# Optimization experiments

Hardware: AMD Instinct MI355X
Metric: run time of the kernel (lower is better)

## Reference

```python
import jax, jax.numpy as jnp
import numpy as np

H = 1024        # hidden_size
V = 50257       # output_size (vocab)
L = 50          # max_length (encoder positions)
N_LAYERS = 2    # python loop count over the shared single-layer GRU


def setup_inputs() -> dict:
    key = jax.random.key(0)
    ks = jax.random.split(key, 16)
    s = 0.02
    return {
        "input_ids": jax.random.randint(ks[0], (1,), 0, V),
        "hidden": jax.random.normal(ks[1], (1, 1, H), jnp.float32),
        "encoder_outputs": jax.random.normal(ks[2], (L, H), jnp.float32),
        # learned parameters
        "emb": jax.random.normal(ks[3], (V, H), jnp.float32) * s,
        "attn_w": jax.random.normal(ks[4], (L, 2 * H), jnp.float32) * s,
        "attn_b": jnp.zeros((L,), jnp.float32),
        "comb_w": jax.random.normal(ks[5], (H, 2 * H), jnp.float32) * s,
        "comb_b": jnp.zeros((H,), jnp.float32),
        "w_ih": jax.random.normal(ks[6], (3 * H, H), jnp.float32) * s,
        "w_hh": jax.random.normal(ks[7], (3 * H, H), jnp.float32) * s,
        "b_ih": jnp.zeros((3 * H,), jnp.float32),
        "b_hh": jnp.zeros((3 * H,), jnp.float32),
        "out_w": jax.random.normal(ks[8], (V, H), jnp.float32) * s,
        "out_b": jnp.zeros((V,), jnp.float32),
    }


def _gru_cell(x, h, w_ih, w_hh, b_ih, b_hh):
    # PyTorch GRU gate order: [r, z, n] stacked along dim 0 of (3H, H) weights.
    gx = w_ih @ x + b_ih
    gh = w_hh @ h + b_hh
    r = jax.nn.sigmoid(gx[:H] + gh[:H])
    z = jax.nn.sigmoid(gx[H:2 * H] + gh[H:2 * H])
    n = jnp.tanh(gx[2 * H:] + r * gh[2 * H:])
    return (1.0 - z) * n + z * h


def reference(input_ids, hidden, encoder_outputs, emb, attn_w, attn_b,
              comb_w, comb_b, w_ih, w_hh, b_ih, b_hh, out_w, out_b):
    # batch=1 single decode step; dropout is identity (eval mode)
    embedded = emb[input_ids[0]]                     # [H]
    h = hidden[0, 0]                                 # [H]
    concat = jnp.concatenate([embedded, h])          # [2H]
    attn_weights = jax.nn.softmax(attn_w @ concat + attn_b)   # [L]
    attn_applied = attn_weights @ encoder_outputs    # [H]  (bmm with batch 1)
    output = comb_w @ jnp.concatenate([embedded, attn_applied]) + comb_b  # [H]
    for _ in range(N_LAYERS):                        # shared-weight GRU called twice
        x = jax.nn.relu(output)
        h = _gru_cell(x, h, w_ih, w_hh, b_ih, b_hh)
        output = h
    log_probs = jax.nn.log_softmax(out_w @ output + out_b)    # [V]
    return log_probs[None, :], h[None, None, :], attn_weights[None, :]
```

## Files before the change

### kernel.cpp

```cpp
#include <hip/hip_runtime.h>
#include <hip/hip_bf16.h>

#define H 1024
#define V 50257
#define L 50

__global__ void scores_kernel(const int* __restrict__ input_ids,
                              const float* __restrict__ hidden,
                              const float* __restrict__ emb,
                              const float* __restrict__ attn_w,
                              const float* __restrict__ attn_b,
                              float* __restrict__ ws_scores) {
    __shared__ float s_part[8];
    const int tid = threadIdx.x;
    const int l   = blockIdx.x;
    const int wave = tid >> 6, lane = tid & 63;
    const int token = input_ids[0];

    float4 a = ((const float4*)(attn_w + (size_t)l * 2 * H))[tid];
    float4 x = (tid < 256) ? ((const float4*)(emb + (size_t)token * H))[tid]
                           : ((const float4*)hidden)[tid - 256];
    float acc = a.x * x.x + a.y * x.y + a.z * x.z + a.w * x.w;
    #pragma unroll
    for (int off = 32; off; off >>= 1) acc += __shfl_down(acc, off);
    if (lane == 0) s_part[wave] = acc;
    __syncthreads();
    if (tid == 0) {
        float s = 0.f;
        #pragma unroll
        for (int w = 0; w < 8; ++w) s += s_part[w];
        ws_scores[l] = s + attn_b[l];
    }
}

__global__ void applied_kernel(const float* __restrict__ ws_scores,
                               const float* __restrict__ enc,
                               float* __restrict__ ws_app,
                               float* __restrict__ out_attnw) {
    const int j = blockIdx.x * 256 + threadIdx.x;
    float w[L];
    float m = ws_scores[0];
    #pragma unroll
    for (int l = 1; l < L; ++l) m = fmaxf(m, ws_scores[l]);
    float s = 0.f;
    #pragma unroll
    for (int l = 0; l < L; ++l) { w[l] = expf(ws_scores[l] - m); s += w[l]; }
    float inv = 1.f / s;
    float acc = 0.f;
    #pragma unroll
    for (int l = 0; l < L; ++l) { w[l] *= inv; acc += w[l] * enc[l * H + j]; }
    ws_app[j] = acc;
    if (blockIdx.x == 0 && threadIdx.x < L) out_attnw[threadIdx.x] = w[threadIdx.x];
}

__global__ void comb_kernel(const float* __restrict__ comb_w,
                            const float* __restrict__ comb_b,
                            const int* __restrict__ input_ids,
                            const float* __restrict__ emb,
                            const float* __restrict__ applied,
                            float* __restrict__ x1) {
    __shared__ __align__(16) float s_c[2 * H];
    const int tid = threadIdx.x;
    const int token = input_ids[0];
    ((float4*)s_c)[tid] = ((const float4*)(emb + (size_t)token * H))[tid];
    ((float4*)(s_c + H))[tid] = ((const float4*)applied)[tid];
    __syncthreads();

    const int wave = tid >> 6, lane = tid & 63;
    const int i = blockIdx.x * 4 + wave;
    const float4* r4 = (const float4*)(comb_w + (size_t)i * 2 * H);
    const float4* c4 = (const float4*)s_c;
    float acc = 0.f;
    #pragma unroll
    for (int kk = 0; kk < 8; ++kk) {
        int k = kk * 64 + lane;
        float4 a = r4[k], b = c4[k];
        acc += a.x * b.x + a.y * b.y + a.z * b.z + a.w * b.w;
    }
    #pragma unroll
    for (int off = 32; off; off >>= 1) acc += __shfl_down(acc, off);
    if (lane == 0) x1[i] = fmaxf(acc + comb_b[i], 0.f);
}

__global__ void gru_kernel(const float* __restrict__ x,
                           const float* __restrict__ hprev,
                           const float* __restrict__ w_ih,
                           const float* __restrict__ w_hh,
                           const float* __restrict__ b_ih,
                           const float* __restrict__ b_hh,
                           float* __restrict__ h_out,
                           float* __restrict__ x_out,
                           float* __restrict__ h_copy)
{
    __shared__ __align__(16) float s_x[H];
    __shared__ __align__(16) float s_h[H];
    const int tid = threadIdx.x;
    ((float4*)s_x)[tid] = ((const float4*)x)[tid];
    ((float4*)s_h)[tid] = ((const float4*)hprev)[tid];
    __syncthreads();

    const int wave = tid >> 6, lane = tid & 63;
    const int i = blockIdx.x * 4 + wave;
    const float4* x4 = (const float4*)s_x;
    const float4* h4 = (const float4*)s_h;
    const float4* wr_x = (const float4*)(w_ih + (size_t)i * H);
    const float4* wz_x = (const float4*)(w_ih + (size_t)(H + i) * H);
    const float4* wn_x = (const float4*)(w_ih + (size_t)(2 * H + i) * H);
    const float4* wr_h = (const float4*)(w_hh + (size_t)i * H);
    const float4* wz_h = (const float4*)(w_hh + (size_t)(H + i) * H);
    const float4* wn_h = (const float4*)(w_hh + (size_t)(2 * H + i) * H);

    float ar = 0.f, az = 0.f, an = 0.f, br = 0.f, bz = 0.f, bn = 0.f;
    #pragma unroll
    for (int kk = 0; kk < 4; ++kk) {
        int k = kk * 64 + lane;
        float4 xv = x4[k], hv = h4[k], t;
        t = wr_x[k]; ar += t.x * xv.x + t.y * xv.y + t.z * xv.z + t.w * xv.w;
        t = wz_x[k]; az += t.x * xv.x + t.y * xv.y + t.z * xv.z + t.w * xv.w;
        t = wn_x[k]; an += t.x * xv.x + t.y * xv.y + t.z * xv.z + t.w * xv.w;
        t = wr_h[k]; br += t.x * hv.x + t.y * hv.y + t.z * hv.z + t.w * hv.w;
        t = wz_h[k]; bz += t.x * hv.x + t.y * hv.y + t.z * hv.z + t.w * hv.w;
        t = wn_h[k]; bn += t.x * hv.x + t.y * hv.y + t.z * hv.z + t.w * hv.w;
    }
    #pragma unroll
    for (int off = 32; off; off >>= 1) {
        ar += __shfl_down(ar, off); az += __shfl_down(az, off);
        an += __shfl_down(an, off); br += __shfl_down(br, off);
        bz += __shfl_down(bz, off); bn += __shfl_down(bn, off);
    }
    if (lane == 0) {
        float gxr = ar + b_ih[i],         ghr = br + b_hh[i];
        float gxz = az + b_ih[H + i],     ghz = bz + b_hh[H + i];
        float gxn = an + b_ih[2 * H + i], ghn = bn + b_hh[2 * H + i];
        float r = 1.f / (1.f + expf(-(gxr + ghr)));
        float z = 1.f / (1.f + expf(-(gxz + ghz)));
        float n = tanhf(gxn + r * ghn);
        float hn = (1.f - z) * n + z * s_h[i];
        h_out[i] = hn;
        if (x_out)  x_out[i]  = fmaxf(hn, 0.f);
        if (h_copy) h_copy[i] = hn;
    }
}

__global__ void logits_kernel(const float* __restrict__ out_w,
                              const float* __restrict__ out_b,
                              const float* __restrict__ h,
                              float* __restrict__ out,
                              float* __restrict__ partials) {
    __shared__ __align__(16) float s_h[H];
    __shared__ float s_part[4];
    const int tid = threadIdx.x;
    ((float4*)s_h)[tid] = ((const float4*)h)[tid];
    __syncthreads();

    const int wave = tid >> 6, lane = tid & 63;
    const float4* h4 = (const float4*)s_h;
    const int v0 = blockIdx.x * 8 + wave * 2;
    const int v1 = v0 + 1;
    float acc0 = 0.f, acc1 = 0.f;
    const float4* w0 = (const float4*)(out_w + (size_t)v0 * H);
    const float4* w1 = (const float4*)(out_w + (size_t)v1 * H);
    if (v1 < V) {
        #pragma unroll
        for (int kk = 0; kk < 4; ++kk) {
            int k = kk * 64 + lane;
            float4 b = h4[k];
            float4 a0 = w0[k], a1 = w1[k];
            acc0 += a0.x * b.x + a0.y * b.y + a0.z * b.z + a0.w * b.w;
            acc1 += a1.x * b.x + a1.y * b.y + a1.z * b.z + a1.w * b.w;
        }
    } else if (v0 < V) {
        #pragma unroll
        for (int kk = 0; kk < 4; ++kk) {
            int k = kk * 64 + lane;
            float4 b = h4[k];
            float4 a0 = w0[k];
            acc0 += a0.x * b.x + a0.y * b.y + a0.z * b.z + a0.w * b.w;
        }
    }
    #pragma unroll
    for (int off = 32; off; off >>= 1) {
        acc0 += __shfl_down(acc0, off);
        acc1 += __shfl_down(acc1, off);
    }
    float psum = 0.f;
    if (lane == 0) {
        if (v0 < V) { float lg = acc0 + out_b[v0]; out[v0] = lg; psum += expf(lg); }
        if (v1 < V) { float lg = acc1 + out_b[v1]; out[v1] = lg; psum += expf(lg); }
        s_part[wave] = psum;
    }
    __syncthreads();
    if (tid == 0)
        partials[blockIdx.x] = s_part[0] + s_part[1] + s_part[2] + s_part[3];
}

__global__ void lse_kernel(const float* __restrict__ partials, int n,
                           float* __restrict__ lse) {
    __shared__ float red[256];
    const int tid = threadIdx.x;
    float s = 0.f;
    for (int i = tid; i < n; i += 256) s += partials[i];
    red[tid] = s;
    __syncthreads();
    for (int off = 128; off; off >>= 1) {
        if (tid < off) red[tid] += red[tid + off];
        __syncthreads();
    }
    if (tid == 0) *lse = logf(red[0]);
}

__global__ void sub_kernel(float* __restrict__ out,
                           const float* __restrict__ lse) {
    const int v = blockIdx.x * 256 + threadIdx.x;
    if (v < V) out[v] -= *lse;
}

extern "C" void kernel_launch(void* const* d_in, const int* in_sizes, int n_in,
                              void* d_out, int out_size, void* d_ws, size_t ws_size,
                              hipStream_t stream) {
    const int*   input_ids = (const int*)d_in[0];
    const float* hidden    = (const float*)d_in[1];
    const float* enc       = (const float*)d_in[2];
    const float* emb       = (const float*)d_in[3];
    const float* attn_w    = (const float*)d_in[4];
    const float* attn_b    = (const float*)d_in[5];
    const float* comb_w    = (const float*)d_in[6];
    const float* comb_b    = (const float*)d_in[7];
    const float* w_ih      = (const float*)d_in[8];
    const float* w_hh      = (const float*)d_in[9];
    const float* b_ih      = (const float*)d_in[10];
    const float* b_hh      = (const float*)d_in[11];
    const float* out_w     = (const float*)d_in[12];
    const float* out_b     = (const float*)d_in[13];

    float* out = (float*)d_out;
    float* ws  = (float*)d_ws;
    float* ws_scores = ws;
    float* ws_app    = ws + 64;
    float* ws_x1     = ws_app + H;
    float* ws_h1     = ws_x1 + H;
    float* ws_x2     = ws_h1 + H;
    float* ws_h2     = ws_x2 + H;
    float* ws_part   = ws_h2 + H;
    float* ws_lse    = ws_part + 6400;

    const int nblk_logits = (V + 7) / 8;

    scores_kernel<<<L, 512, 0, stream>>>(input_ids, hidden, emb, attn_w, attn_b,
                                         ws_scores);
    applied_kernel<<<4, 256, 0, stream>>>(ws_scores, enc, ws_app, out + V + H);
    comb_kernel<<<256, 256, 0, stream>>>(comb_w, comb_b, input_ids, emb, ws_app,
                                         ws_x1);
    gru_kernel<<<256, 256, 0, stream>>>(ws_x1, hidden, w_ih, w_hh, b_ih, b_hh,
                                        ws_h1, ws_x2, nullptr);
    gru_kernel<<<256, 256, 0, stream>>>(ws_x2, ws_h1, w_ih, w_hh, b_ih, b_hh,
                                        ws_h2, nullptr, out + V);
    logits_kernel<<<nblk_logits, 256, 0, stream>>>(out_w, out_b, ws_h2,
                                                   out, ws_part);
    lse_kernel<<<1, 256, 0, stream>>>(ws_part, nblk_logits, ws_lse);
    sub_kernel<<<(V + 255) / 256, 256, 0, stream>>>(out, ws_lse);
}
```

Before: 430.6 us.

## Fuse attention into combine kernel, widen GRU grid, four rows per logits wave

Merges the attention scores, softmax, weighted encoder sum and combine GEMV into one kernel. Each of the 256 blocks recomputes the 50 scores and the encoder sum redundantly, which saves two launches but repeats that work and re-reads attn_w and enc in every block. The GRU kernel now uses one output row per block across 1024 blocks, with a cross-wave shared-memory reduction. The logits kernel has each wave compute four vocab rows instead of two, which halves the block count and adds loads in flight per wave.

```diff
diff --git a/kernel.cpp b/kernel.cpp
--- a/kernel.cpp
+++ b/kernel.cpp
@@ -5,81 +5,79 @@
 #define V 50257
 #define L 50
 
-__global__ void scores_kernel(const int* __restrict__ input_ids,
-                              const float* __restrict__ hidden,
-                              const float* __restrict__ emb,
-                              const float* __restrict__ attn_w,
-                              const float* __restrict__ attn_b,
-                              float* __restrict__ ws_scores) {
-    __shared__ float s_part[8];
-    const int tid = threadIdx.x;
-    const int l   = blockIdx.x;
+__global__ void attn_comb_kernel(const int* __restrict__ input_ids,
+                                 const float* __restrict__ hidden,
+                                 const float* __restrict__ enc,
+                                 const float* __restrict__ emb,
+                                 const float* __restrict__ attn_w,
+                                 const float* __restrict__ attn_b,
+                                 const float* __restrict__ comb_w,
+                                 const float* __restrict__ comb_b,
+                                 float* __restrict__ x1,
+                                 float* __restrict__ out_attnw) {
+    __shared__ __align__(16) float s_c[2 * H];
+    __shared__ float s_sc[64];
+    __shared__ float s_w[64];
+    const int tid = threadIdx.x;
     const int wave = tid >> 6, lane = tid & 63;
     const int token = input_ids[0];
 
-    float4 a = ((const float4*)(attn_w + (size_t)l * 2 * H))[tid];
-    float4 x = (tid < 256) ? ((const float4*)(emb + (size_t)token * H))[tid]
-                           : ((const float4*)hidden)[tid - 256];
-    float acc = a.x * x.x + a.y * x.y + a.z * x.z + a.w * x.w;
-    #pragma unroll
-    for (int off = 32; off; off >>= 1) acc += __shfl_down(acc, off);
-    if (lane == 0) s_part[wave] = acc;
-    __syncthreads();
+    float4* sc4 = (float4*)s_c;
+    sc4[tid]       = ((const float4*)(emb + (size_t)token * H))[tid];
+    sc4[256 + tid] = ((const float4*)hidden)[tid];
+    __syncthreads();
+
+    for (int l = wave; l < L; l += 4) {
+        const float4* r4 = (const float4*)(attn_w + (size_t)l * 2 * H);
+        float acc = 0.f;
+        #pragma unroll
+        for (int kk = 0; kk < 8; ++kk) {
+            int k = kk * 64 + lane;
+            float4 a = r4[k], b = sc4[k];
+            acc += a.x * b.x + a.y * b.y + a.z * b.z + a.w * b.w;
+        }
+        #pragma unroll
+        for (int off = 32; off; off >>= 1) acc += __shfl_down(acc, off);
+        if (lane == 0) s_sc[l] = acc + attn_b[l];
+    }
+    __syncthreads();
+
     if (tid == 0) {
+        float m = s_sc[0];
+        for (int l = 1; l < L; ++l) m = fmaxf(m, s_sc[l]);
         float s = 0.f;
-        #pragma unroll
-        for (int w = 0; w < 8; ++w) s += s_part[w];
-        ws_scores[l] = s + attn_b[l];
-    }
-}
-
-__global__ void applied_kernel(const float* __restrict__ ws_scores,
-                               const float* __restrict__ enc,
-                               float* __restrict__ ws_app,
-                               float* __restrict__ out_attnw) {
-    const int j = blockIdx.x * 256 + threadIdx.x;
-    float w[L];
-    float m = ws_scores[0];
-    #pragma unroll
-    for (int l = 1; l < L; ++l) m = fmaxf(m, ws_scores[l]);
-    float s = 0.f;
-    #pragma unroll
-    for (int l = 0; l < L; ++l) { w[l] = expf(ws_scores[l] - m); s += w[l]; }
-    float inv = 1.f / s;
-    float acc = 0.f;
-    #pragma unroll
-    for (int l = 0; l < L; ++l) { w[l] *= inv; acc += w[l] * enc[l * H + j]; }
-    ws_app[j] = acc;
-    if (blockIdx.x == 0 && threadIdx.x < L) out_attnw[threadIdx.x] = w[threadIdx.x];
-}
-
-__global__ void comb_kernel(const float* __restrict__ comb_w,
-                            const float* __restrict__ comb_b,
-                            const int* __restrict__ input_ids,
-                            const float* __restrict__ emb,
-                            const float* __restrict__ applied,
-                            float* __restrict__ x1) {
-    __shared__ __align__(16) float s_c[2 * H];
-    const int tid = threadIdx.x;
-    const int token = input_ids[0];
-    ((float4*)s_c)[tid] = ((const float4*)(emb + (size_t)token * H))[tid];
-    ((float4*)(s_c + H))[tid] = ((const float4*)applied)[tid];
-    __syncthreads();
-
-    const int wave = tid >> 6, lane = tid & 63;
-    const int i = blockIdx.x * 4 + wave;
-    const float4* r4 = (const float4*)(comb_w + (size_t)i * 2 * H);
-    const float4* c4 = (const float4*)s_c;
-    float acc = 0.f;
-    #pragma unroll
-    for (int kk = 0; kk < 8; ++kk) {
-        int k = kk * 64 + lane;
-        float4 a = r4[k], b = c4[k];
-        acc += a.x * b.x + a.y * b.y + a.z * b.z + a.w * b.w;
-    }
-    #pragma unroll
-    for (int off = 32; off; off >>= 1) acc += __shfl_down(acc, off);
-    if (lane == 0) x1[i] = fmaxf(acc + comb_b[i], 0.f);
+        for (int l = 0; l < L; ++l) { float e = expf(s_sc[l] - m); s_w[l] = e; s += e; }
+        float inv = 1.f / s;
+        for (int l = 0; l < L; ++l) s_w[l] *= inv;
+    }
+    __syncthreads();
+
+    {
+        float4 acc4 = make_float4(0.f, 0.f, 0.f, 0.f);
+        for (int l = 0; l < L; ++l) {
+            float w = s_w[l];
+            float4 v = ((const float4*)enc)[l * 256 + tid];
+            acc4.x += w * v.x; acc4.y += w * v.y; acc4.z += w * v.z; acc4.w += w * v.w;
+        }
+        sc4[256 + tid] = acc4;
+        if (blockIdx.x == 0 && tid < L) out_attnw[tid] = s_w[tid];
+    }
+    __syncthreads();
+
+    {
+        const int r = blockIdx.x * 4 + wave;
+        const float4* wr = (const float4*)(comb_w + (size_t)r * 2 * H);
+        float acc = 0.f;
+        #pragma unroll
+        for (int kk = 0; kk < 8; ++kk) {
+            int k = kk * 64 + lane;
+            float4 a = wr[k], b = sc4[k];
+            acc += a.x * b.x + a.y * b.y + a.z * b.z + a.w * b.w;
+        }
+        #pragma unroll
+        for (int off = 32; off; off >>= 1) acc += __shfl_down(acc, off);
+        if (lane == 0) x1[r] = fmaxf(acc + comb_b[r], 0.f);
+    }
 }
 
 __global__ void gru_kernel(const float* __restrict__ x,
@@ -92,50 +90,53 @@
                            float* __restrict__ x_out,
                            float* __restrict__ h_copy)
 {
-    __shared__ __align__(16) float s_x[H];
-    __shared__ __align__(16) float s_h[H];
-    const int tid = threadIdx.x;
-    ((float4*)s_x)[tid] = ((const float4*)x)[tid];
-    ((float4*)s_h)[tid] = ((const float4*)hprev)[tid];
-    __syncthreads();
-
+    __shared__ float s_red[4][8];
+    const int tid = threadIdx.x;
     const int wave = tid >> 6, lane = tid & 63;
-    const int i = blockIdx.x * 4 + wave;
-    const float4* x4 = (const float4*)s_x;
-    const float4* h4 = (const float4*)s_h;
-    const float4* wr_x = (const float4*)(w_ih + (size_t)i * H);
-    const float4* wz_x = (const float4*)(w_ih + (size_t)(H + i) * H);
-    const float4* wn_x = (const float4*)(w_ih + (size_t)(2 * H + i) * H);
-    const float4* wr_h = (const float4*)(w_hh + (size_t)i * H);
-    const float4* wz_h = (const float4*)(w_hh + (size_t)(H + i) * H);
-    const float4* wn_h = (const float4*)(w_hh + (size_t)(2 * H + i) * H);
-
-    float ar = 0.f, az = 0.f, an = 0.f, br = 0.f, bz = 0.f, bn = 0.f;
-    #pragma unroll
-    for (int kk = 0; kk < 4; ++kk) {
-        int k = kk * 64 + lane;
-        float4 xv = x4[k], hv = h4[k], t;
-        t = wr_x[k]; ar += t.x * xv.x + t.y * xv.y + t.z * xv.z + t.w * xv.w;
-        t = wz_x[k]; az += t.x * xv.x + t.y * xv.y + t.z * xv.z + t.w * xv.w;
-        t = wn_x[k]; an += t.x * xv.x + t.y * xv.y + t.z * xv.z + t.w * xv.w;
-        t = wr_h[k]; br += t.x * hv.x + t.y * hv.y + t.z * hv.z + t.w * hv.w;
-        t = wz_h[k]; bz += t.x * hv.x + t.y * hv.y + t.z * hv.z + t.w * hv.w;
-        t = wn_h[k]; bn += t.x * hv.x + t.y * hv.y + t.z * hv.z + t.w * hv.w;
-    }
+    const int i = blockIdx.x;
+    const int k = wave * 64 + lane;
+
+    float4 xv = ((const float4*)x)[k];
+    float4 hv = ((const float4*)hprev)[k];
+    const float4* m0 = (const float4*)(w_ih + (size_t)i * H);
+    const float4* m1 = (const float4*)(w_ih + (size_t)(H + i) * H);
+    const float4* m2 = (const float4*)(w_ih + (size_t)(2 * H + i) * H);
+    const float4* m3 = (const float4*)(w_hh + (size_t)i * H);
+    const float4* m4 = (const float4*)(w_hh + (size_t)(H + i) * H);
+    const float4* m5 = (const float4*)(w_hh + (size_t)(2 * H + i) * H);
+    float4 t;
+    float a0, a1, a2, a3, a4, a5;
+    t = m0[k]; a0 = t.x * xv.x + t.y * xv.y + t.z * xv.z + t.w * xv.w;
+    t = m1[k]; a1 = t.x * xv.x + t.y * xv.y + t.z * xv.z + t.w * xv.w;
+    t = m2[k]; a2 = t.x * xv.x + t.y * xv.y + t.z * xv.z + t.w * xv.w;
+    t = m3[k]; a3 = t.x * hv.x + t.y * hv.y + t.z * hv.z + t.w * hv.w;
+    t = m4[k]; a4 = t.x * hv.x + t.y * hv.y + t.z * hv.z + t.w * hv.w;
+    t = m5[k]; a5 = t.x * hv.x + t.y * hv.y + t.z * hv.z + t.w * hv.w;
     #pragma unroll
     for (int off = 32; off; off >>= 1) {
-        ar += __shfl_down(ar, off); az += __shfl_down(az, off);
-        an += __shfl_down(an, off); br += __shfl_down(br, off);
-        bz += __shfl_down(bz, off); bn += __shfl_down(bn, off);
+        a0 += __shfl_down(a0, off); a1 += __shfl_down(a1, off);
+        a2 += __shfl_down(a2, off); a3 += __shfl_down(a3, off);
+        a4 += __shfl_down(a4, off); a5 += __shfl_down(a5, off);
     }
     if (lane == 0) {
-        float gxr = ar + b_ih[i],         ghr = br + b_hh[i];
-        float gxz = az + b_ih[H + i],     ghz = bz + b_hh[H + i];
-        float gxn = an + b_ih[2 * H + i], ghn = bn + b_hh[2 * H + i];
+        s_red[wave][0] = a0; s_red[wave][1] = a1; s_red[wave][2] = a2;
+        s_red[wave][3] = a3; s_red[wave][4] = a4; s_red[wave][5] = a5;
+    }
+    __syncthreads();
+    if (tid == 0) {
+        float g0 = 0, g1 = 0, g2 = 0, g3 = 0, g4 = 0, g5 = 0;
+        #pragma unroll
+        for (int w = 0; w < 4; ++w) {
+            g0 += s_red[w][0]; g1 += s_red[w][1]; g2 += s_red[w][2];
+            g3 += s_red[w][3]; g4 += s_red[w][4]; g5 += s_red[w][5];
+        }
+        float gxr = g0 + b_ih[i],         ghr = g3 + b_hh[i];
+        float gxz = g1 + b_ih[H + i],     ghz = g4 + b_hh[H + i];
+        float gxn = g2 + b_ih[2 * H + i], ghn = g5 + b_hh[2 * H + i];
         float r = 1.f / (1.f + expf(-(gxr + ghr)));
         float z = 1.f / (1.f + expf(-(gxz + ghz)));
         float n = tanhf(gxn + r * ghn);
-        float hn = (1.f - z) * n + z * s_h[i];
+        float hn = (1.f - z) * n + z * hprev[i];
         h_out[i] = hn;
         if (x_out)  x_out[i]  = fmaxf(hn, 0.f);
         if (h_copy) h_copy[i] = hn;
@@ -155,38 +156,55 @@
 
     const int wave = tid >> 6, lane = tid & 63;
     const float4* h4 = (const float4*)s_h;
-    const int v0 = blockIdx.x * 8 + wave * 2;
-    const int v1 = v0 + 1;
-    float acc0 = 0.f, acc1 = 0.f;
-    const float4* w0 = (const float4*)(out_w + (size_t)v0 * H);
-    const float4* w1 = (const float4*)(out_w + (size_t)v1 * H);
-    if (v1 < V) {
+    const int rbase = blockIdx.x * 16 + wave * 4;
+    float acc[4] = {0.f, 0.f, 0.f, 0.f};
+
+    if (rbase + 3 < V) {
+        const float4* w0 = (const float4*)(out_w + (size_t)rbase * H);
+        const float4* w1 = (const float4*)(out_w + (size_t)(rbase + 1) * H);
+        const float4* w2 = (const float4*)(out_w + (size_t)(rbase + 2) * H);
+        const float4* w3 = (const float4*)(out_w + (size_t)(rbase + 3) * H);
         #pragma unroll
         for (int kk = 0; kk < 4; ++kk) {
             int k = kk * 64 + lane;
             float4 b = h4[k];
-            float4 a0 = w0[k], a1 = w1[k];
-            acc0 += a0.x * b.x + a0.y * b.y + a0.z * b.z + a0.w * b.w;
-            acc1 += a1.x * b.x + a1.y * b.y + a1.z * b.z + a1.w * b.w;
-        }
-    } else if (v0 < V) {
-        #pragma unroll
-        for (int kk = 0; kk < 4; ++kk) {
-            int k = kk * 64 + lane;
-            float4 b = h4[k];
-            float4 a0 = w0[k];
-            acc0 += a0.x * b.x + a0.y * b.y + a0.z * b.z + a0.w * b.w;
+            float4 a0 = w0[k], a1 = w1[k], a2 = w2[k], a3 = w3[k];
+            acc[0] += a0.x * b.x + a0.y * b.y + a0.z * b.z + a0.w * b.w;
+            acc[1] += a1.x * b.x + a1.y * b.y + a1.z * b.z + a1.w * b.w;
+            acc[2] += a2.x * b.x + a2.y * b.y + a2.z * b.z + a2.w * b.w;
+            acc[3] += a3.x * b.x + a3.y * b.y + a3.z * b.z + a3.w * b.w;
+        }
+    } else {
+        #pragma unroll
+        for (int r = 0; r < 4; ++r) {
+            if (rbase + r < V) {
+                const float4* wr = (const float4*)(out_w + (size_t)(rbase + r) * H);
+                #pragma unroll
+                for (int kk = 0; kk < 4; ++kk) {
+                    int k = kk * 64 + lane;
+                    float4 b = h4[k];
+                    float4 a = wr[k];
+                    acc[r] += a.x * b.x + a.y * b.y + a.z * b.z + a.w * b.w;
+                }
+            }
         }
     }
     #pragma unroll
     for (int off = 32; off; off >>= 1) {
-        acc0 += __shfl_down(acc0, off);
-        acc1 += __shfl_down(acc1, off);
-    }
-    float psum = 0.f;
+        acc[0] += __shfl_down(acc[0], off); acc[1] += __shfl_down(acc[1], off);
+        acc[2] += __shfl_down(acc[2], off); acc[3] += __shfl_down(acc[3], off);
+    }
     if (lane == 0) {
-        if (v0 < V) { float lg = acc0 + out_b[v0]; out[v0] = lg; psum += expf(lg); }
-        if (v1 < V) { float lg = acc1 + out_b[v1]; out[v1] = lg; psum += expf(lg); }
+        float psum = 0.f;
+        #pragma unroll
+        for (int r = 0; r < 4; ++r) {
+            int v = rbase + r;
+            if (v < V) {
+                float lg = acc[r] + out_b[v];
+                out[v] = lg;
+                psum += expf(lg);
+            }
+        }
         s_part[wave] = psum;
     }
     __syncthreads();
@@ -235,26 +253,22 @@
 
     float* out = (float*)d_out;
     float* ws  = (float*)d_ws;
-    float* ws_scores = ws;
-    float* ws_app    = ws + 64;
-    float* ws_x1     = ws_app + H;
-    float* ws_h1     = ws_x1 + H;
-    float* ws_x2     = ws_h1 + H;
-    float* ws_h2     = ws_x2 + H;
-    float* ws_part   = ws_h2 + H;
-    float* ws_lse    = ws_part + 6400;
-
-    const int nblk_logits = (V + 7) / 8;
-
-    scores_kernel<<<L, 512, 0, stream>>>(input_ids, hidden, emb, attn_w, attn_b,
-                                         ws_scores);
-    applied_kernel<<<4, 256, 0, stream>>>(ws_scores, enc, ws_app, out + V + H);
-    comb_kernel<<<256, 256, 0, stream>>>(comb_w, comb_b, input_ids, emb, ws_app,
-                                         ws_x1);
-    gru_kernel<<<256, 256, 0, stream>>>(ws_x1, hidden, w_ih, w_hh, b_ih, b_hh,
-                                        ws_h1, ws_x2, nullptr);
-    gru_kernel<<<256, 256, 0, stream>>>(ws_x2, ws_h1, w_ih, w_hh, b_ih, b_hh,
-                                        ws_h2, nullptr, out + V);
+    float* ws_x1   = ws;
+    float* ws_h1   = ws + 1024;
+    float* ws_x2   = ws + 2048;
+    float* ws_h2   = ws + 3072;
+    float* ws_part = ws + 4096;
+    float* ws_lse  = ws_part + 3200;
+
+    const int nblk_logits = (V + 15) / 16;
+
+    attn_comb_kernel<<<256, 256, 0, stream>>>(input_ids, hidden, enc, emb,
+                                              attn_w, attn_b, comb_w, comb_b,
+                                              ws_x1, out + V + H);
+    gru_kernel<<<1024, 256, 0, stream>>>(ws_x1, hidden, w_ih, w_hh, b_ih, b_hh,
+                                         ws_h1, ws_x2, nullptr);
+    gru_kernel<<<1024, 256, 0, stream>>>(ws_x2, ws_h1, w_ih, w_hh, b_ih, b_hh,
+                                         ws_h2, nullptr, out + V);
     logits_kernel<<<nblk_logits, 256, 0, stream>>>(out_w, out_b, ws_h2,
                                                    out, ws_part);
     lse_kernel<<<1, 256, 0, stream>>>(ws_part, nblk_logits, ws_lse);
```

Measured after the change: 437.0 us. About the same (+1.5%).
